# Kernel optimization log

Hardware: AMD Instinct MI355X
Metric: run time of the kernel (lower is better)

Reference implementation:

```python
import jax, jax.numpy as jnp
import numpy as np

B, C, KC, H, W = 8, 256, 32, 128, 128


def setup_inputs() -> dict:
    key = jax.random.key(0)
    ks = jax.random.split(key, 5)
    x = jax.random.normal(ks[0], (B, C, H, W), dtype=jnp.float32)
    Wq = jax.random.normal(ks[1], (KC, C), dtype=jnp.float32) / np.sqrt(C)
    Wk = jax.random.normal(ks[2], (KC, C), dtype=jnp.float32) / np.sqrt(C)
    Wv = jax.random.normal(ks[3], (C, C), dtype=jnp.float32) / np.sqrt(C)
    bq = jnp.zeros((KC,), dtype=jnp.float32)
    bk = jnp.zeros((KC,), dtype=jnp.float32)
    bv = jnp.zeros((C,), dtype=jnp.float32)
    gamma = jax.random.uniform(ks[4], (1,), dtype=jnp.float32)
    return {"x": x, "Wq": Wq, "bq": bq, "Wk": Wk, "bk": bk, "Wv": Wv, "bv": bv, "gamma": gamma}


def reference(x, Wq, bq, Wk, bk, Wv, bv, gamma):
    b, c, h, w = x.shape
    n = h * w
    xf = x.reshape(b, c, n)  # [B,C,N]
    # 1x1 convs == per-pixel linear maps
    q = jnp.einsum('kc,bcn->bkn', Wq, xf) + bq[None, :, None]
    k = jnp.einsum('kc,bcn->bkn', Wk, xf) + bk[None, :, None]
    v = jnp.einsum('vc,bcn->bvn', Wv, xf) + bv[None, :, None]
    fm = lambda t: jax.nn.elu(t) + 1.0  # elu+1 feature map
    qm = fm(q)  # [B,KC,N]
    km = fm(k)  # [B,KC,N]
    kv = jnp.einsum('bkn,bvn->bkv', km, v)          # kv context [B,KC,C]
    z = km.sum(axis=-1)                              # z norm factor [B,KC]
    qkv = jnp.einsum('bkn,bkv->bnv', qm, kv)        # [B,N,C]
    qz = jnp.einsum('bkn,bk->bn', qm, z)            # [B,N]
    normed = qkv / jnp.maximum(qz, 1e-6)[..., None]  # [B,N,C]
    out = normed.transpose(0, 2, 1).reshape(b, c, h, w)
    return gamma[0] * out + x
```

## Files before the change

kernel.cpp:

```cpp
#include <hip/hip_runtime.h>

#define Bn  8
#define Cn  256
#define KCn 32
#define Nn  16384
#define CW  512
#define NCH (Nn / CW)

typedef __attribute__((ext_vector_type(8))) short bf16x8;
typedef __attribute__((ext_vector_type(4))) short short4v;
typedef __attribute__((ext_vector_type(4))) float f32x4;

__device__ __forceinline__ float elup1(float v) {
    return v > 0.0f ? v + 1.0f : __expf(v);
}
__device__ __forceinline__ short f2bf(float f) {
    unsigned u = __float_as_uint(f);
    return (short)((u + 0x7FFFu + ((u >> 16) & 1u)) >> 16);
}

__global__ void k_prep(const float* __restrict__ Wk, const float* __restrict__ Wq,
                       unsigned short* __restrict__ Wkbf, unsigned short* __restrict__ Wqbf) {
    const int i = blockIdx.x * 512 + threadIdx.x;
    Wkbf[i] = (unsigned short)f2bf(Wk[i]);
    Wqbf[i] = (unsigned short)f2bf(Wq[i]);
}

__global__ __launch_bounds__(512, 4) void k_km_S(const float* __restrict__ x,
                                                 const unsigned short* __restrict__ Wkbf,
                                                 const float* __restrict__ bk,
                                                 float* __restrict__ S,
                                                 float* __restrict__ Zpart) {
    __shared__ short kml[KCn][520];
    __shared__ float zred[8][KCn];

    const int t = threadIdx.x, b = blockIdx.y, n0 = blockIdx.x * CW;
    const int lane = t & 63, wv = t >> 6;
    const int g = lane >> 4, l15 = lane & 15;
    const int pxw = wv * 64;
    const float* xb = x + (size_t)b * Cn * Nn;

    f32x4 acc1[2][4] = {};
    for (int kc = 0; kc < 8; ++kc) {
        float xf[4][8];
#pragma unroll
        for (int nt = 0; nt < 4; ++nt) {
            const float* bp = xb + (size_t)(kc * 32 + g * 8) * Nn + n0 + pxw + nt * 16 + l15;
#pragma unroll
            for (int j = 0; j < 8; ++j) xf[nt][j] = bp[(size_t)j * Nn];
        }
        const bf16x8 wa0 = *(const bf16x8*)(Wkbf + l15 * Cn + kc * 32 + g * 8);
        const bf16x8 wa1 = *(const bf16x8*)(Wkbf + (16 + l15) * Cn + kc * 32 + g * 8);
#pragma unroll
        for (int nt = 0; nt < 4; ++nt) {
            bf16x8 bf;
#pragma unroll
            for (int j = 0; j < 8; ++j) bf[j] = f2bf(xf[nt][j]);
            acc1[0][nt] = __builtin_amdgcn_mfma_f32_16x16x32_bf16(wa0, bf, acc1[0][nt], 0, 0, 0);
            acc1[1][nt] = __builtin_amdgcn_mfma_f32_16x16x32_bf16(wa1, bf, acc1[1][nt], 0, 0, 0);
        }
    }

#pragma unroll
    for (int mt = 0; mt < 2; ++mt)
#pragma unroll
        for (int j = 0; j < 4; ++j) {
            const int kf = mt * 16 + g * 4 + j;
            const float bkv = bk[kf];
            float s = 0.f;
#pragma unroll
            for (int nt = 0; nt < 4; ++nt) {
                const float v = elup1(acc1[mt][nt][j] + bkv);
                kml[kf][pxw + nt * 16 + l15] = f2bf(v);
                s += v;
            }
            s += __shfl_xor(s, 1); s += __shfl_xor(s, 2);
            s += __shfl_xor(s, 4); s += __shfl_xor(s, 8);
            if (l15 == 0) zred[wv][kf] = s;
        }
    __syncthreads();
    if (t < KCn) {
        float s = 0.f;
#pragma unroll
        for (int w = 0; w < 8; ++w) s += zred[w][t];
        Zpart[((size_t)b * NCH + blockIdx.x) * KCn + t] = s;
    }

    f32x4 acc2[2][2] = {};
    const int crow = wv * 32;
#pragma unroll 2
    for (int ks = 0; ks < 16; ++ks) {
        bf16x8 a2[2];
#pragma unroll
        for (int mt = 0; mt < 2; ++mt) {
            const float* ap = xb + (size_t)(crow + mt * 16 + l15) * Nn + n0 + ks * 32 + g * 8;
            const float4 f0 = *(const float4*)ap;
            const float4 f1 = *(const float4*)(ap + 4);
            bf16x8 v;
            v[0] = f2bf(f0.x); v[1] = f2bf(f0.y); v[2] = f2bf(f0.z); v[3] = f2bf(f0.w);
            v[4] = f2bf(f1.x); v[5] = f2bf(f1.y); v[6] = f2bf(f1.z); v[7] = f2bf(f1.w);
            a2[mt] = v;
        }
        const bf16x8 b20 = *(const bf16x8*)&kml[l15][ks * 32 + g * 8];
        const bf16x8 b21 = *(const bf16x8*)&kml[16 + l15][ks * 32 + g * 8];
        acc2[0][0] = __builtin_amdgcn_mfma_f32_16x16x32_bf16(a2[0], b20, acc2[0][0], 0, 0, 0);
        acc2[0][1] = __builtin_amdgcn_mfma_f32_16x16x32_bf16(a2[0], b21, acc2[0][1], 0, 0, 0);
        acc2[1][0] = __builtin_amdgcn_mfma_f32_16x16x32_bf16(a2[1], b20, acc2[1][0], 0, 0, 0);
        acc2[1][1] = __builtin_amdgcn_mfma_f32_16x16x32_bf16(a2[1], b21, acc2[1][1], 0, 0, 0);
    }
    float* Sb = S + (size_t)b * Cn * KCn;
#pragma unroll
    for (int mt = 0; mt < 2; ++mt)
#pragma unroll
        for (int nt = 0; nt < 2; ++nt)
#pragma unroll
            for (int j = 0; j < 4; ++j)
                atomicAdd(&Sb[(crow + mt * 16 + g * 4 + j) * KCn + nt * 16 + l15],
                          acc2[mt][nt][j]);
}

__global__ __launch_bounds__(256) void k_kv(const float* __restrict__ Wv,
                                            const float* __restrict__ bv,
                                            const float* __restrict__ S,
                                            const float* __restrict__ Zpart,
                                            float* __restrict__ Zf,
                                            unsigned short* __restrict__ KVT) {
    __shared__ float Sl[Cn][KCn];
    __shared__ float zl[KCn];
    const int t = threadIdx.x;
    const int b = blockIdx.y;
    const int vc0 = blockIdx.x * 32;
    const float* Sb = S + (size_t)b * Cn * KCn;
#pragma unroll
    for (int i = 0; i < 32; ++i) ((float*)Sl)[i * 256 + t] = Sb[i * 256 + t];
    if (t < KCn) {
        float s = 0.f;
#pragma unroll 8
        for (int ch = 0; ch < NCH; ++ch) s += Zpart[((size_t)b * NCH + ch) * KCn + t];
        zl[t] = s;
        if (blockIdx.x == 0) Zf[b * KCn + t] = s;
    }
    __syncthreads();
    const int vc = vc0 + (t >> 3);
    const int kq = (t & 7) * 4;
    const float bvv = bv[vc];
    f32x4 acc;
#pragma unroll
    for (int i = 0; i < 4; ++i) acc[i] = bvv * zl[kq + i];
    const float* wv = Wv + (size_t)vc * Cn;
#pragma unroll 4
    for (int c = 0; c < Cn; ++c) {
        const float w = wv[c];
        const f32x4 s4 = *(const f32x4*)&Sl[c][kq];
#pragma unroll
        for (int i = 0; i < 4; ++i) acc[i] += w * s4[i];
    }
    unsigned short* kp = KVT + ((size_t)b * Cn + vc) * KCn + kq;
    ushort4 o;
    o.x = (unsigned short)f2bf(acc[0]); o.y = (unsigned short)f2bf(acc[1]);
    o.z = (unsigned short)f2bf(acc[2]); o.w = (unsigned short)f2bf(acc[3]);
    *(ushort4*)kp = o;
}

__global__ __launch_bounds__(512, 4) void k_out(const float* __restrict__ x,
                                                const unsigned short* __restrict__ Wqbf,
                                                const float* __restrict__ bq,
                                                const unsigned short* __restrict__ KVT,
                                                const float* __restrict__ Zf,
                                                const float* __restrict__ gamma,
                                                float* __restrict__ out) {
    __shared__ short qml[CW][40];
    __shared__ short kvtl[Cn][40];

    const int t = threadIdx.x, b = blockIdx.y, n0 = blockIdx.x * CW;
    const int lane = t & 63, wv = t >> 6;
    const int g = lane >> 4, l15 = lane & 15;
    const int pxw = wv * 64;
    const float* xb = x + (size_t)b * Cn * Nn;

    {
        const int vc = t >> 1, half = t & 1;
        const bf16x8* src = (const bf16x8*)(KVT + ((size_t)b * Cn + vc) * KCn + half * 16);
        *(bf16x8*)&kvtl[vc][half * 16]     = src[0];
        *(bf16x8*)&kvtl[vc][half * 16 + 8] = src[1];
    }
    __syncthreads();

    f32x4 acc1[2][4] = {};
    for (int kc = 0; kc < 8; ++kc) {
        float xf[4][8];
#pragma unroll
        for (int nt = 0; nt < 4; ++nt) {
            const float* bp = xb + (size_t)(kc * 32 + g * 8) * Nn + n0 + pxw + nt * 16 + l15;
#pragma unroll
            for (int j = 0; j < 8; ++j) xf[nt][j] = bp[(size_t)j * Nn];
        }
        const bf16x8 wa0 = *(const bf16x8*)(Wqbf + l15 * Cn + kc * 32 + g * 8);
        const bf16x8 wa1 = *(const bf16x8*)(Wqbf + (16 + l15) * Cn + kc * 32 + g * 8);
#pragma unroll
        for (int nt = 0; nt < 4; ++nt) {
            bf16x8 bf;
#pragma unroll
            for (int j = 0; j < 8; ++j) bf[j] = f2bf(xf[nt][j]);
            acc1[0][nt] = __builtin_amdgcn_mfma_f32_16x16x32_bf16(wa0, bf, acc1[0][nt], 0, 0, 0);
            acc1[1][nt] = __builtin_amdgcn_mfma_f32_16x16x32_bf16(wa1, bf, acc1[1][nt], 0, 0, 0);
        }
    }

#pragma unroll
    for (int mt = 0; mt < 2; ++mt)
#pragma unroll
        for (int nt = 0; nt < 4; ++nt) {
            short4v q4;
#pragma unroll
            for (int j = 0; j < 4; ++j)
                q4[j] = f2bf(elup1(acc1[mt][nt][j] + bq[mt * 16 + g * 4 + j]));
            *(short4v*)&qml[pxw + nt * 16 + l15][mt * 16 + g * 4] = q4;
        }

    bf16x8 qb[4];
#pragma unroll
    for (int nt = 0; nt < 4; ++nt)
        qb[nt] = *(const bf16x8*)&qml[pxw + nt * 16 + l15][g * 8];

    bf16x8 az = {};
    if (l15 == 0) {
#pragma unroll
        for (int j = 0; j < 8; ++j) az[j] = f2bf(Zf[b * KCn + g * 8 + j]);
    }
    const float gm = gamma[0];
    float r[4];
#pragma unroll
    for (int nt = 0; nt < 4; ++nt) {
        f32x4 u = {};
        u = __builtin_amdgcn_mfma_f32_16x16x32_bf16(az, qb[nt], u, 0, 0, 0);
        const float qz = __shfl(u[0], l15);
        r[nt] = gm / fmaxf(qz, 1e-6f);
    }

    const float* xr = xb + n0 + pxw;
    float* ob = out + (size_t)b * Cn * Nn + n0 + pxw;
#pragma unroll 2
    for (int mt = 0; mt < 16; ++mt) {
        const bf16x8 a = *(const bf16x8*)&kvtl[mt * 16 + l15][g * 8];
#pragma unroll
        for (int nt = 0; nt < 4; ++nt) {
            f32x4 c0 = {};
            c0 = __builtin_amdgcn_mfma_f32_16x16x32_bf16(a, qb[nt], c0, 0, 0, 0);
#pragma unroll
            for (int j = 0; j < 4; ++j) {
                const size_t ro = (size_t)(mt * 16 + g * 4 + j) * Nn + nt * 16 + l15;
                ob[ro] = c0[j] * r[nt] + xr[ro];
            }
        }
    }
}

extern "C" void kernel_launch(void* const* d_in, const int* in_sizes, int n_in,
                              void* d_out, int out_size, void* d_ws, size_t ws_size,
                              hipStream_t stream) {
    const float* x     = (const float*)d_in[0];
    const float* Wq    = (const float*)d_in[1];
    const float* bq    = (const float*)d_in[2];
    const float* Wk    = (const float*)d_in[3];
    const float* bk    = (const float*)d_in[4];
    const float* Wv    = (const float*)d_in[5];
    const float* bv    = (const float*)d_in[6];
    const float* gamma = (const float*)d_in[7];
    float* out = (float*)d_out;

    float* S     = (float*)d_ws;
    float* Zpart = S + (size_t)Bn * Cn * KCn;
    float* Zf    = Zpart + (size_t)Bn * NCH * KCn;
    unsigned short* KVT  = (unsigned short*)(Zf + (size_t)Bn * KCn);
    unsigned short* Wkbf = KVT + (size_t)Bn * Cn * KCn;
    unsigned short* Wqbf = Wkbf + (size_t)KCn * Cn;

    hipMemsetAsync(d_ws, 0,
                   ((size_t)Bn * Cn * KCn + (size_t)Bn * NCH * KCn) * sizeof(float),
                   stream);
    k_prep<<<dim3(16), 512, 0, stream>>>(Wk, Wq, Wkbf, Wqbf);
    k_km_S<<<dim3(NCH, Bn), 512, 0, stream>>>(x, Wkbf, bk, S, Zpart);
    k_kv  <<<dim3(8, Bn), 256, 0, stream>>>(Wv, bv, S, Zpart, Zf, KVT);
    k_out <<<dim3(NCH, Bn), 512, 0, stream>>>(x, Wqbf, bq, KVT, Zf, gamma, out);
}
```

Baseline: 388.1 us.

## Compute Q features in first pass and stage output through LDS for coalesced stores

```diff
diff --git a/kernel.cpp b/kernel.cpp
--- a/kernel.cpp
+++ b/kernel.cpp
@@ -4,11 +4,10 @@
 #define Cn  256
 #define KCn 32
 #define Nn  16384
-#define CW  512
+#define CW  256
 #define NCH (Nn / CW)
 
 typedef __attribute__((ext_vector_type(8))) short bf16x8;
-typedef __attribute__((ext_vector_type(4))) short short4v;
 typedef __attribute__((ext_vector_type(4))) float f32x4;
 
 __device__ __forceinline__ float elup1(float v) {
@@ -18,46 +17,55 @@
     unsigned u = __float_as_uint(f);
     return (short)((u + 0x7FFFu + ((u >> 16) & 1u)) >> 16);
 }
-
-__global__ void k_prep(const float* __restrict__ Wk, const float* __restrict__ Wq,
-                       unsigned short* __restrict__ Wkbf, unsigned short* __restrict__ Wqbf) {
-    const int i = blockIdx.x * 512 + threadIdx.x;
-    Wkbf[i] = (unsigned short)f2bf(Wk[i]);
-    Wqbf[i] = (unsigned short)f2bf(Wq[i]);
+__device__ __forceinline__ bf16x8 cvt8(const float* __restrict__ p) {
+    const float4 f0 = *(const float4*)p;
+    const float4 f1 = *(const float4*)(p + 4);
+    bf16x8 v;
+    v[0] = f2bf(f0.x); v[1] = f2bf(f0.y); v[2] = f2bf(f0.z); v[3] = f2bf(f0.w);
+    v[4] = f2bf(f1.x); v[5] = f2bf(f1.y); v[6] = f2bf(f1.z); v[7] = f2bf(f1.w);
+    return v;
 }
 
 __global__ __launch_bounds__(512, 4) void k_km_S(const float* __restrict__ x,
-                                                 const unsigned short* __restrict__ Wkbf,
+                                                 const float* __restrict__ Wk,
+                                                 const float* __restrict__ Wq,
                                                  const float* __restrict__ bk,
+                                                 const float* __restrict__ bq,
                                                  float* __restrict__ S,
-                                                 float* __restrict__ Zpart) {
-    __shared__ short kml[KCn][520];
+                                                 float* __restrict__ Zpart,
+                                                 unsigned short* __restrict__ qml) {
+    __shared__ short kml[KCn][264];
     __shared__ float zred[8][KCn];
 
     const int t = threadIdx.x, b = blockIdx.y, n0 = blockIdx.x * CW;
     const int lane = t & 63, wv = t >> 6;
     const int g = lane >> 4, l15 = lane & 15;
-    const int pxw = wv * 64;
+    const int pxw = wv * 32;
     const float* xb = x + (size_t)b * Cn * Nn;
 
-    f32x4 acc1[2][4] = {};
+    f32x4 akm[2][2] = {}, aqm[2][2] = {};
     for (int kc = 0; kc < 8; ++kc) {
-        float xf[4][8];
-#pragma unroll
-        for (int nt = 0; nt < 4; ++nt) {
-            const float* bp = xb + (size_t)(kc * 32 + g * 8) * Nn + n0 + pxw + nt * 16 + l15;
+        const int c0 = kc * 32 + g * 8;
+        const bf16x8 wk0 = cvt8(Wk + l15 * Cn + c0);
+        const bf16x8 wk1 = cvt8(Wk + (16 + l15) * Cn + c0);
+        const bf16x8 wq0 = cvt8(Wq + l15 * Cn + c0);
+        const bf16x8 wq1 = cvt8(Wq + (16 + l15) * Cn + c0);
+        float xf[2][8];
+#pragma unroll
+        for (int nt = 0; nt < 2; ++nt) {
+            const float* bp = xb + (size_t)c0 * Nn + n0 + pxw + nt * 16 + l15;
 #pragma unroll
             for (int j = 0; j < 8; ++j) xf[nt][j] = bp[(size_t)j * Nn];
         }
-        const bf16x8 wa0 = *(const bf16x8*)(Wkbf + l15 * Cn + kc * 32 + g * 8);
-        const bf16x8 wa1 = *(const bf16x8*)(Wkbf + (16 + l15) * Cn + kc * 32 + g * 8);
-#pragma unroll
-        for (int nt = 0; nt < 4; ++nt) {
+#pragma unroll
+        for (int nt = 0; nt < 2; ++nt) {
             bf16x8 bf;
 #pragma unroll
             for (int j = 0; j < 8; ++j) bf[j] = f2bf(xf[nt][j]);
-            acc1[0][nt] = __builtin_amdgcn_mfma_f32_16x16x32_bf16(wa0, bf, acc1[0][nt], 0, 0, 0);
-            acc1[1][nt] = __builtin_amdgcn_mfma_f32_16x16x32_bf16(wa1, bf, acc1[1][nt], 0, 0, 0);
+            akm[0][nt] = __builtin_amdgcn_mfma_f32_16x16x32_bf16(wk0, bf, akm[0][nt], 0, 0, 0);
+            akm[1][nt] = __builtin_amdgcn_mfma_f32_16x16x32_bf16(wk1, bf, akm[1][nt], 0, 0, 0);
+            aqm[0][nt] = __builtin_amdgcn_mfma_f32_16x16x32_bf16(wq0, bf, aqm[0][nt], 0, 0, 0);
+            aqm[1][nt] = __builtin_amdgcn_mfma_f32_16x16x32_bf16(wq1, bf, aqm[1][nt], 0, 0, 0);
         }
     }
 
@@ -66,13 +74,16 @@
 #pragma unroll
         for (int j = 0; j < 4; ++j) {
             const int kf = mt * 16 + g * 4 + j;
-            const float bkv = bk[kf];
+            const float bkv = bk[kf], bqv = bq[kf];
             float s = 0.f;
 #pragma unroll
-            for (int nt = 0; nt < 4; ++nt) {
-                const float v = elup1(acc1[mt][nt][j] + bkv);
-                kml[kf][pxw + nt * 16 + l15] = f2bf(v);
+            for (int nt = 0; nt < 2; ++nt) {
+                const int px = pxw + nt * 16 + l15;
+                const float v = elup1(akm[mt][nt][j] + bkv);
+                kml[kf][px] = f2bf(v);
                 s += v;
+                const float q = elup1(aqm[mt][nt][j] + bqv);
+                qml[((size_t)b * KCn + kf) * Nn + n0 + px] = (unsigned short)f2bf(q);
             }
             s += __shfl_xor(s, 1); s += __shfl_xor(s, 2);
             s += __shfl_xor(s, 4); s += __shfl_xor(s, 8);
@@ -89,18 +100,11 @@
     f32x4 acc2[2][2] = {};
     const int crow = wv * 32;
 #pragma unroll 2
-    for (int ks = 0; ks < 16; ++ks) {
+    for (int ks = 0; ks < 8; ++ks) {
         bf16x8 a2[2];
 #pragma unroll
-        for (int mt = 0; mt < 2; ++mt) {
-            const float* ap = xb + (size_t)(crow + mt * 16 + l15) * Nn + n0 + ks * 32 + g * 8;
-            const float4 f0 = *(const float4*)ap;
-            const float4 f1 = *(const float4*)(ap + 4);
-            bf16x8 v;
-            v[0] = f2bf(f0.x); v[1] = f2bf(f0.y); v[2] = f2bf(f0.z); v[3] = f2bf(f0.w);
-            v[4] = f2bf(f1.x); v[5] = f2bf(f1.y); v[6] = f2bf(f1.z); v[7] = f2bf(f1.w);
-            a2[mt] = v;
-        }
+        for (int mt = 0; mt < 2; ++mt)
+            a2[mt] = cvt8(xb + (size_t)(crow + mt * 16 + l15) * Nn + n0 + ks * 32 + g * 8);
         const bf16x8 b20 = *(const bf16x8*)&kml[l15][ks * 32 + g * 8];
         const bf16x8 b21 = *(const bf16x8*)&kml[16 + l15][ks * 32 + g * 8];
         acc2[0][0] = __builtin_amdgcn_mfma_f32_16x16x32_bf16(a2[0], b20, acc2[0][0], 0, 0, 0);
@@ -163,19 +167,18 @@
 }
 
 __global__ __launch_bounds__(512, 4) void k_out(const float* __restrict__ x,
-                                                const unsigned short* __restrict__ Wqbf,
-                                                const float* __restrict__ bq,
+                                                const unsigned short* __restrict__ qml,
                                                 const unsigned short* __restrict__ KVT,
                                                 const float* __restrict__ Zf,
                                                 const float* __restrict__ gamma,
                                                 float* __restrict__ out) {
-    __shared__ short qml[CW][40];
     __shared__ short kvtl[Cn][40];
+    __shared__ float stagef[2][16][260];
 
     const int t = threadIdx.x, b = blockIdx.y, n0 = blockIdx.x * CW;
     const int lane = t & 63, wv = t >> 6;
     const int g = lane >> 4, l15 = lane & 15;
-    const int pxw = wv * 64;
+    const int pxw = wv * 32;
     const float* xb = x + (size_t)b * Cn * Nn;
 
     {
@@ -184,44 +187,15 @@
         *(bf16x8*)&kvtl[vc][half * 16]     = src[0];
         *(bf16x8*)&kvtl[vc][half * 16 + 8] = src[1];
     }
-    __syncthreads();
-
-    f32x4 acc1[2][4] = {};
-    for (int kc = 0; kc < 8; ++kc) {
-        float xf[4][8];
-#pragma unroll
-        for (int nt = 0; nt < 4; ++nt) {
-            const float* bp = xb + (size_t)(kc * 32 + g * 8) * Nn + n0 + pxw + nt * 16 + l15;
-#pragma unroll
-            for (int j = 0; j < 8; ++j) xf[nt][j] = bp[(size_t)j * Nn];
-        }
-        const bf16x8 wa0 = *(const bf16x8*)(Wqbf + l15 * Cn + kc * 32 + g * 8);
-        const bf16x8 wa1 = *(const bf16x8*)(Wqbf + (16 + l15) * Cn + kc * 32 + g * 8);
-#pragma unroll
-        for (int nt = 0; nt < 4; ++nt) {
-            bf16x8 bf;
-#pragma unroll
-            for (int j = 0; j < 8; ++j) bf[j] = f2bf(xf[nt][j]);
-            acc1[0][nt] = __builtin_amdgcn_mfma_f32_16x16x32_bf16(wa0, bf, acc1[0][nt], 0, 0, 0);
-            acc1[1][nt] = __builtin_amdgcn_mfma_f32_16x16x32_bf16(wa1, bf, acc1[1][nt], 0, 0, 0);
-        }
-    }
-
-#pragma unroll
-    for (int mt = 0; mt < 2; ++mt)
-#pragma unroll
-        for (int nt = 0; nt < 4; ++nt) {
-            short4v q4;
-#pragma unroll
-            for (int j = 0; j < 4; ++j)
-                q4[j] = f2bf(elup1(acc1[mt][nt][j] + bq[mt * 16 + g * 4 + j]));
-            *(short4v*)&qml[pxw + nt * 16 + l15][mt * 16 + g * 4] = q4;
-        }
-
-    bf16x8 qb[4];
-#pragma unroll
-    for (int nt = 0; nt < 4; ++nt)
-        qb[nt] = *(const bf16x8*)&qml[pxw + nt * 16 + l15][g * 8];
+
+    bf16x8 qb[2];
+#pragma unroll
+    for (int nt = 0; nt < 2; ++nt) {
+        const unsigned short* qp = qml + (size_t)b * KCn * Nn + n0 + pxw + nt * 16 + l15;
+#pragma unroll
+        for (int j = 0; j < 8; ++j)
+            qb[nt][j] = (short)qp[(size_t)(g * 8 + j) * Nn];
+    }
 
     bf16x8 az = {};
     if (l15 == 0) {
@@ -229,30 +203,45 @@
         for (int j = 0; j < 8; ++j) az[j] = f2bf(Zf[b * KCn + g * 8 + j]);
     }
     const float gm = gamma[0];
-    float r[4];
-#pragma unroll
-    for (int nt = 0; nt < 4; ++nt) {
+    float r[2];
+#pragma unroll
+    for (int nt = 0; nt < 2; ++nt) {
         f32x4 u = {};
         u = __builtin_amdgcn_mfma_f32_16x16x32_bf16(az, qb[nt], u, 0, 0, 0);
         const float qz = __shfl(u[0], l15);
         r[nt] = gm / fmaxf(qz, 1e-6f);
     }
-
-    const float* xr = xb + n0 + pxw;
-    float* ob = out + (size_t)b * Cn * Nn + n0 + pxw;
-#pragma unroll 2
+    __syncthreads();
+
+    const int srow = t >> 5, scol = (t & 31) * 4;
+    int buf = 0;
     for (int mt = 0; mt < 16; ++mt) {
-        const bf16x8 a = *(const bf16x8*)&kvtl[mt * 16 + l15][g * 8];
-#pragma unroll
-        for (int nt = 0; nt < 4; ++nt) {
+#pragma unroll
+        for (int nt = 0; nt < 2; ++nt) {
+            const bf16x8 a = *(const bf16x8*)&kvtl[mt * 16 + l15][g * 8];
             f32x4 c0 = {};
             c0 = __builtin_amdgcn_mfma_f32_16x16x32_bf16(a, qb[nt], c0, 0, 0, 0);
 #pragma unroll
-            for (int j = 0; j < 4; ++j) {
-                const size_t ro = (size_t)(mt * 16 + g * 4 + j) * Nn + nt * 16 + l15;
-                ob[ro] = c0[j] * r[nt] + xr[ro];
+            for (int j = 0; j < 4; ++j)
+                stagef[buf][g * 4 + j][pxw + nt * 16 + l15] = c0[j] * r[nt];
+        }
+        __syncthreads();
+        {
+            const int vc = mt * 16 + srow;
+            const float* xr = xb + (size_t)vc * Nn + n0;
+            float* ob = out + ((size_t)b * Cn + vc) * Nn + n0;
+#pragma unroll
+            for (int k = 0; k < 2; ++k) {
+                const int col = scol + k * 128;
+                const float4 sv = *(const float4*)&stagef[buf][srow][col];
+                const float4 xv = *(const float4*)(xr + col);
+                float4 o;
+                o.x = sv.x + xv.x; o.y = sv.y + xv.y;
+                o.z = sv.z + xv.z; o.w = sv.w + xv.w;
+                *(float4*)(ob + col) = o;
             }
         }
+        buf ^= 1;
     }
 }
 
@@ -272,15 +261,13 @@
     float* S     = (float*)d_ws;
     float* Zpart = S + (size_t)Bn * Cn * KCn;
     float* Zf    = Zpart + (size_t)Bn * NCH * KCn;
-    unsigned short* KVT  = (unsigned short*)(Zf + (size_t)Bn * KCn);
-    unsigned short* Wkbf = KVT + (size_t)Bn * Cn * KCn;
-    unsigned short* Wqbf = Wkbf + (size_t)KCn * Cn;
+    unsigned short* KVT = (unsigned short*)(Zf + (size_t)Bn * KCn);
+    unsigned short* qml = KVT + (size_t)Bn * Cn * KCn;
 
     hipMemsetAsync(d_ws, 0,
                    ((size_t)Bn * Cn * KCn + (size_t)Bn * NCH * KCn) * sizeof(float),
                    stream);
-    k_prep<<<dim3(16), 512, 0, stream>>>(Wk, Wq, Wkbf, Wqbf);
-    k_km_S<<<dim3(NCH, Bn), 512, 0, stream>>>(x, Wkbf, bk, S, Zpart);
+    k_km_S<<<dim3(NCH, Bn), 512, 0, stream>>>(x, Wk, Wq, bk, bq, S, Zpart, qml);
     k_kv  <<<dim3(8, Bn), 256, 0, stream>>>(Wv, bv, S, Zpart, Zf, KVT);
-    k_out <<<dim3(NCH, Bn), 512, 0, stream>>>(x, Wqbf, bq, KVT, Zf, gamma, out);
-}
+    k_out <<<dim3(NCH, Bn), 512, 0, stream>>>(x, qml, KVT, Zf, gamma, out);
+}
```

Result: faster. 322.8 us (-16.8%).
